# Performance work log

Hardware: AMD Instinct MI355X
Metric: run time of the kernel (lower is better)

## Reference

```python
import jax, jax.numpy as jnp
import numpy as np

N = 10000        # nodes
E = 160000       # graph edges (avg degree 16)
EI = 100000      # interaction edges
EP = 50000       # positive interaction edges
EA = 50000       # a2b edges
H, D = 4, 128    # GAT heads, per-head (and per-layer) dim
F_IN, F_EDGE = 39, 27   # 17+19+3 node feats, 27 edge feats
EMB = 256
FCN_IN = F_IN + 3 * D + D  # 551: x stacked with 3 GAT outputs + GCN output

PARAM_SHAPES = []
for l, fin in enumerate([F_IN, D, D]):
    PARAM_SHAPES += [(f"gat{l}_W", (fin, H * D)), (f"gat{l}_We", (F_EDGE, H * D)),
                     (f"gat{l}_asrc", (H, D)), (f"gat{l}_adst", (H, D)),
                     (f"gat{l}_aedge", (H, D)), (f"gat{l}_b", (D,))]
PARAM_SHAPES += [("gcn_W", (D, D)), ("gcn_b", (D,))]
for nm, fi, hh, fo in [("fcn", FCN_IN, 1024, EMB), ("link", 2 * EMB + 2, 1024, 1),
                       ("a2b", 2 * EMB, 1024, 6), ("node", EMB, 1024, 16),
                       ("int", 2 * EMB + 2, 1024, 3)]:
    PARAM_SHAPES += [(f"{nm}_W1", (fi, hh)), (f"{nm}_b1", (hh,)),
                     (f"{nm}_g", (hh,)), (f"{nm}_be", (hh,)),
                     (f"{nm}_W2", (hh, fo)), (f"{nm}_b2", (fo,))]
PARAM_NAMES = [n for n, _ in PARAM_SHAPES]


def setup_inputs():
    ks = jax.random.split(jax.random.key(0), len(PARAM_SHAPES) + 10)
    inp = {
        "x": jax.random.normal(ks[0], (N, F_IN), jnp.float32),
        "edge_index": jax.random.randint(ks[1], (2, E), 0, N),
        "edge_attr": jax.random.normal(ks[2], (E, F_EDGE), jnp.float32),
        "interaction_edge_index_pos": jax.random.randint(ks[3], (2, EP), 0, N),
        "interaction_edge_index": jax.random.randint(ks[4], (2, EI), 0, N),
        "xyz_data": jax.random.normal(ks[5], (N, 3), jnp.float32),
        "vector_data": jax.random.normal(ks[6], (N, 3), jnp.float32),
        "a2b_index": jax.random.randint(ks[7], (2, EA), 0, N),
        "mask": jnp.zeros((1,), jnp.float32),  # only used by the (disabled) evolver path
    }
    for i, (name, shp) in enumerate(PARAM_SHAPES):
        if name.endswith("_g"):
            inp[name] = jnp.ones(shp, jnp.float32)        # BatchNorm gamma
        elif name.endswith(("_be", "_b", "_b1", "_b2")):
            inp[name] = jnp.zeros(shp, jnp.float32)       # biases / BN beta
        else:
            inp[name] = jax.random.normal(ks[10 + i], shp, jnp.float32) * 0.05
    return inp


def _bn(h, g, b, eps=1e-5):
    # BatchNorm1d in training mode: biased batch statistics over axis 0
    m = h.mean(0)
    v = ((h - m) ** 2).mean(0)
    return (h - m) * jax.lax.rsqrt(v + eps) * g + b


def _seg_softmax(logits, seg, n):
    m = jax.ops.segment_max(logits, seg, num_segments=n)
    e = jnp.exp(logits - m[seg])
    s = jax.ops.segment_sum(e, seg, num_segments=n)
    return e / (s[seg] + 1e-16)


def _cos(a, b, eps=1e-8):
    na = jnp.maximum(jnp.sqrt((a * a).sum(1)), eps)
    nb = jnp.maximum(jnp.sqrt((b * b).sum(1)), eps)
    return (a * b).sum(1) / (na * nb)


def _forward(x, edge_attr, xyz_data, vector_data, edge_index, iep, iei, a2b_index, params):
    p = dict(zip(PARAM_NAMES, params))
    n = x.shape[0]
    src, dst = edge_index[0], edge_index[1]
    loops = jnp.arange(n)
    # GATConv add_self_loops with fill_value='mean': per-node mean of incoming edge_attr
    cnt = jax.ops.segment_sum(jnp.ones(src.shape[0], x.dtype), dst, num_segments=n)
    loop_attr = jax.ops.segment_sum(edge_attr, dst, num_segments=n) / jnp.maximum(cnt, 1.0)[:, None]
    src_a = jnp.concatenate([src, loops])
    dst_a = jnp.concatenate([dst, loops])
    ea_a = jnp.concatenate([edge_attr, loop_attr], 0)

    def gat(xx, W, We, asrc, adst, aedge, b):
        h = (xx @ W).reshape(n, H, D)
        a_s = (h * asrc).sum(-1)                               # [n,H]
        a_d = (h * adst).sum(-1)                               # [n,H]
        a_e = ((ea_a @ We).reshape(-1, H, D) * aedge).sum(-1)  # [E',H]
        alpha = jax.nn.leaky_relu(a_s[src_a] + a_d[dst_a] + a_e, 0.2)
        alpha = _seg_softmax(alpha, dst_a, n)                  # softmax over incoming edges
        out = jax.ops.segment_sum(h[src_a] * alpha[:, :, None], dst_a, num_segments=n)
        return out.mean(1) + b                                 # concat=False -> mean over heads

    out = x
    steps = [x]
    for l in range(3):
        out = jax.nn.relu(gat(out, p[f"gat{l}_W"], p[f"gat{l}_We"], p[f"gat{l}_asrc"],
                              p[f"gat{l}_adst"], p[f"gat{l}_aedge"], p[f"gat{l}_b"]))
        steps.append(out)
    # GCNConv: self loops (weight 1) + symmetric normalization
    deg = jax.ops.segment_sum(jnp.ones(dst_a.shape[0], x.dtype), dst_a, num_segments=n)
    dinv = jnp.where(deg > 0, deg ** -0.5, 0.0)
    norm = dinv[src_a] * dinv[dst_a]
    hg = out @ p["gcn_W"]
    out = jax.ops.segment_sum(hg[src_a] * norm[:, None], dst_a, num_segments=n) + p["gcn_b"]
    steps.append(out)

    feat = jnp.concatenate(steps, 1)                           # [n, 551]
    h = jax.nn.relu(feat @ p["fcn_W1"] + p["fcn_b1"])
    h = _bn(h, p["fcn_g"], p["fcn_be"])
    emb = jax.nn.relu(h @ p["fcn_W2"] + p["fcn_b2"])           # [n, 256]

    def head(z, nm):
        hh = jax.nn.relu(z @ p[f"{nm}_W1"] + p[f"{nm}_b1"])
        hh = _bn(hh, p[f"{nm}_g"], p[f"{nm}_be"])
        return hh @ p[f"{nm}_W2"] + p[f"{nm}_b2"]

    def pair_feat(idx):
        z = jnp.concatenate([emb[idx[0]], emb[idx[1]]], 1)
        d = ((xyz_data[idx[0]] - xyz_data[idx[1]]) ** 2).sum(1)  # squared distance (no sqrt)
        a = _cos(vector_data[idx[0]], vector_data[idx[1]])
        return jnp.concatenate([z, d[:, None], a[:, None]], 1)

    link_preds = head(pair_feat(iei), "link")
    a2b_preds = head(jnp.concatenate([emb[a2b_index[0]], emb[a2b_index[1]]], 1), "a2b")
    node_preds = head(emb, "node")
    int_preds = head(pair_feat(iep), "int")
    return (link_preds, a2b_preds, node_preds, int_preds)


def reference(x, edge_index, edge_attr, interaction_edge_index_pos, interaction_edge_index,
              xyz_data, vector_data, a2b_index, mask,
              gat0_W, gat0_We, gat0_asrc, gat0_adst, gat0_aedge, gat0_b,
              gat1_W, gat1_We, gat1_asrc, gat1_adst, gat1_aedge, gat1_b,
              gat2_W, gat2_We, gat2_asrc, gat2_adst, gat2_aedge, gat2_b,
              gcn_W, gcn_b,
              fcn_W1, fcn_b1, fcn_g, fcn_be, fcn_W2, fcn_b2,
              link_W1, link_b1, link_g, link_be, link_W2, link_b2,
              a2b_W1, a2b_b1, a2b_g, a2b_be, a2b_W2, a2b_b2,
              node_W1, node_b1, node_g, node_be, node_W2, node_b2,
              int_W1, int_b1, int_g, int_be, int_W2, int_b2):
    loc = locals()
    params = tuple(loc[nm] for nm in PARAM_NAMES)
    return _forward(x, edge_attr, xyz_data, vector_data, edge_index,
                    interaction_edge_index_pos, interaction_edge_index, a2b_index, params)
```

## Files before the change

### kernel.cpp

```cpp
#include <hip/hip_runtime.h>
#include <hip/hip_bf16.h>
#include <cstdint>
#include <cstddef>

typedef __attribute__((ext_vector_type(8))) short bf16x8;
typedef __attribute__((ext_vector_type(4))) float f32x4;

__device__ inline float bf2f(unsigned short u) {
    union { float f; unsigned int i; } c; c.i = ((unsigned int)u) << 16; return c.f;
}
__device__ inline unsigned short f2b(float v) {
    __hip_bfloat16 h = __float2bfloat16(v);
    union { __hip_bfloat16 b; unsigned short u; } c; c.b = h; return c.u;
}

__device__ inline float wmax64(float v) {
    #pragma unroll
    for (int o = 32; o; o >>= 1) v = fmaxf(v, __shfl_xor(v, o));
    return v;
}
__device__ inline float wsum64(float v) {
    #pragma unroll
    for (int o = 32; o; o >>= 1) v += __shfl_xor(v, o);
    return v;
// ... 156 lines not shown
        float l0 = a_s[s * 4 + 0] + d0 + a_e[(size_t)eid * 4 + 0];
        float l1 = a_s[s * 4 + 1] + d1 + a_e[(size_t)eid * 4 + 1];
        float l2 = a_s[s * 4 + 2] + d2 + a_e[(size_t)eid * 4 + 2];
        float l3 = a_s[s * 4 + 3] + d3 + a_e[(size_t)eid * 4 + 3];
        l0 = l0 > 0.f ? l0 : 0.2f * l0;
        l1 = l1 > 0.f ? l1 : 0.2f * l1;
        l2 = l2 > 0.f ? l2 : 0.2f * l2;
        l3 = l3 > 0.f ? l3 : 0.2f * l3;
        m0 = fmaxf(m0, l0); m1 = fmaxf(m1, l1); m2 = fmaxf(m2, l2); m3 = fmaxf(m3, l3);
    }
    m0 = wmax64(m0); m1 = wmax64(m1); m2 = wmax64(m2); m3 = wmax64(m3);
    float s0 = 0, s1 = 0, s2 = 0, s3 = 0;
    for (int e = lane; e < total; e += 64) {
        int eid, s;
        if (e < cnt) { eid = ceid[beg + e]; s = esrc[eid]; } else { eid = E_ + i; s = i; }
        float l0 = a_s[s * 4 + 0] + d0 + a_e[(size_t)eid * 4 + 0];
        float l1 = a_s[s * 4 + 1] + d1 + a_e[(size_t)eid * 4 + 1];
        float l2 = a_s[s * 4 + 2] + d2 + a_e[(size_t)eid * 4 + 2];
        float l3 = a_s[s * 4 + 3] + d3 + a_e[(size_t)eid * 4 + 3];
        l0 = l0 > 0.f ? l0 : 0.2f * l0;
        l1 = l1 > 0.f ? l1 : 0.2f * l1;
        l2 = l2 > 0.f ? l2 : 0.2f * l2;
        l3 = l3 > 0.f ? l3 : 0.2f * l3;
        s0 += __expf(l0 - m0); s1 += __expf(l1 - m1);
        s2 += __expf(l2 - m2); s3 += __expf(l3 - m3);
    }
    s0 = wsum64(s0); s1 = wsum64(s1); s2 = wsum64(s2); s3 = wsum64(s3);
    const int myh = lane >> 4;
    const float mm = myh == 0 ? m0 : myh == 1 ? m1 : myh == 2 ? m2 : m3;
    const float sv = myh == 0 ? s0 : myh == 1 ? s1 : myh == 2 ? s2 : s3;
    const float dd = myh == 0 ? d0 : myh == 1 ? d1 : myh == 2 ? d2 : d3;
    const float iv = 1.f / (sv + 1e-16f);
    float acc[8] = {0, 0, 0, 0, 0, 0, 0, 0};
    for (int e = 0; e < total; ++e) {
        int eid, s;
        if (e < cnt) { eid = ceid[beg + e]; s = esrc[eid]; } else { eid = E_ + i; s = i; }
        float l = a_s[s * 4 + myh] + dd + a_e[(size_t)eid * 4 + myh];
        l = l > 0.f ? l : 0.2f * l;
        const float wgt = __expf(l - mm) * iv;
        union { uint4 u; unsigned short us[8]; } c;
        c.u = *(const uint4*)(hb + (size_t)s * 512 + lane * 8);
        #pragma unroll
        for (int j = 0; j < 8; ++j) acc[j] += wgt * bf2f(c.us[j]);
    }
    __shared__ float sh[512];
    #pragma unroll
    for (int j = 0; j < 8; ++j) sh[lane * 8 + j] = acc[j];
    __syncthreads();
    #pragma unroll
    for (int r = 0; r < 2; ++r) {
        int d = lane * 2 + r;
        float v = 0.25f * (sh[d] + sh[128 + d] + sh[256 + d] + sh[384 + d]) + bvec[d];
        feat[(size_t)i * 551 + colofs + d] = fmaxf(v, 0.f);
    }
}

__global__ __launch_bounds__(64) void k_gcn(const unsigned short* __restrict__ hg, const int* __restrict__ esrc,
    const int* __restrict__ coff, const int* __restrict__ ceid, const int* __restrict__ indeg,
    const float* __restrict__ bvec, float* __restrict__ feat) {
    const int i = blockIdx.x;
    const int lane = threadIdx.x;
    const int beg = coff[i];
    const int cnt = coff[i + 1] - beg;
    const float di = rsqrtf((float)(indeg[i] + 1));
    const int d = lane * 2;
    unsigned int u0 = *(const unsigned int*)(hg + (size_t)i * 128 + d);
    float acc0 = bf2f((unsigned short)(u0 & 0xffff)) * di;
    float acc1 = bf2f((unsigned short)(u0 >> 16)) * di;
    for (int e = 0; e < cnt; ++e) {
        int eid = ceid[beg + e];
        int s = esrc[eid];
        float ds = rsqrtf((float)(indeg[s] + 1));
        unsigned int u = *(const unsigned int*)(hg + (size_t)s * 128 + d);
        acc0 += bf2f((unsigned short)(u & 0xffff)) * ds;
// ... 119 lines not shown
    for (int ch = 0; ch < nch; ++ch) {
        s += tmp[(size_t)ch * 2048 + c];
        ss += tmp[(size_t)ch * 2048 + 1024 + c];
    }
    float m = s / (float)M;
    float v = ss / (float)M - m * m;
    mv[c] = m;
    mv[1024 + c] = fmaxf(v, 0.f);
}

__global__ __launch_bounds__(256) void k_fold(const float* __restrict__ W2, const float* __restrict__ g,
    const float* __restrict__ be, const float* __restrict__ b2, const float* __restrict__ mv,
    float* __restrict__ W2f, float* __restrict__ b2f, int NO) {
    const int c = blockIdx.x;
    const int t = threadIdx.x;
    __shared__ float red[256];
    float accb = 0.f;
    for (int k = t; k < 1024; k += 256) {
        float s = (1.f / sqrtf(mv[1024 + k] + 1e-5f)) * g[k];
        float wv = W2[(size_t)k * NO + c];
        W2f[(size_t)k * NO + c] = wv * s;
        accb += (be[k] - mv[k] * s) * wv;
    }
    red[t] = accb;
    __syncthreads();
    for (int o = 128; o; o >>= 1) {
        if (t < o) red[t] += red[t + o];
        __syncthreads();
    }
    if (t == 0) b2f[c] = b2[c] + red[0];
}

template<bool HASEX>
__global__ __launch_bounds__(256) void k_pairA(
    const unsigned short* __restrict__ u0, const unsigned short* __restrict__ u1, int ldu,
    const float* __restrict__ b1, const float* __restrict__ W1ex,
    const int4* __restrict__ spp,
    int P, float* __restrict__ part) {
    const int b = blockIdx.x, t = threadIdx.x;
    const int chunk = (P + 1023) / 1024;
    const int r0 = b * chunk;
    const int r1 = min(P, r0 + chunk);
    const float4 bb = *(const float4*)(b1 + t * 4);
    float4 wd = make_float4(0, 0, 0, 0), wa = make_float4(0, 0, 0, 0);
    if constexpr (HASEX) {
        wd = *(const float4*)(W1ex + t * 4);
        wa = *(const float4*)(W1ex + 1024 + t * 4);
    }
    float s[4] = {0, 0, 0, 0}, ss[4] = {0, 0, 0, 0};
    int r = r0;
    for (; r + 1 < r1; r += 2) {
        const int4 rA = spp[r], rB = spp[r + 1];
        const int i0A = rA.x, i1A = rA.y, i0B = rB.x, i1B = rB.y;
        float dA = 0, aA = 0, dB = 0, aB = 0;
        if constexpr (HASEX) {
            dA = __int_as_float(rA.z); aA = __int_as_float(rA.w);
            dB = __int_as_float(rB.z); aB = __int_as_float(rB.w);
        }
        const ushort4 q0A = *(const ushort4*)(u0 + (size_t)i0A * ldu + t * 4);
        const ushort4 q1A = *(const ushort4*)(u1 + (size_t)i1A * ldu + t * 4);
        const ushort4 q0B = *(const ushort4*)(u0 + (size_t)i0B * ldu + t * 4);
        const ushort4 q1B = *(const ushort4*)(u1 + (size_t)i1B * ldu + t * 4);
        float hA[4], hB[4];
        hA[0] = bf2f(q0A.x) + bf2f(q1A.x) + bb.x;
        hA[1] = bf2f(q0A.y) + bf2f(q1A.y) + bb.y;
        hA[2] = bf2f(q0A.z) + bf2f(q1A.z) + bb.z;
        hA[3] = bf2f(q0A.w) + bf2f(q1A.w) + bb.w;
        hB[0] = bf2f(q0B.x) + bf2f(q1B.x) + bb.x;
        hB[1] = bf2f(q0B.y) + bf2f(q1B.y) + bb.y;
        hB[2] = bf2f(q0B.z) + bf2f(q1B.z) + bb.z;
        hB[3] = bf2f(q0B.w) + bf2f(q1B.w) + bb.w;
        if constexpr (HASEX) {
            hA[0] += dA * wd.x + aA * wa.x; hA[1] += dA * wd.y + aA * wa.y;
            hA[2] += dA * wd.z + aA * wa.z; hA[3] += dA * wd.w + aA * wa.w;
            hB[0] += dB * wd.x + aB * wa.x; hB[1] += dB * wd.y + aB * wa.y;
            hB[2] += dB * wd.z + aB * wa.z; hB[3] += dB * wd.w + aB * wa.w;
        }
        #pragma unroll
        for (int j = 0; j < 4; ++j) {
            float hvA = fmaxf(hA[j], 0.f);
            float hvB = fmaxf(hB[j], 0.f);
            s[j] += hvA + hvB; ss[j] += hvA * hvA + hvB * hvB;
        }
    }
    if (r < r1) {
        const int4 rA = spp[r];
        const int i0 = rA.x, i1 = rA.y;
        float d = 0, a = 0;
        if constexpr (HASEX) { d = __int_as_float(rA.z); a = __int_as_float(rA.w); }
        const ushort4 q0 = *(const ushort4*)(u0 + (size_t)i0 * ldu + t * 4);
        const ushort4 q1 = *(const ushort4*)(u1 + (size_t)i1 * ldu + t * 4);
        float h[4];
        h[0] = bf2f(q0.x) + bf2f(q1.x) + bb.x;
        h[1] = bf2f(q0.y) + bf2f(q1.y) + bb.y;
        h[2] = bf2f(q0.z) + bf2f(q1.z) + bb.z;
        h[3] = bf2f(q0.w) + bf2f(q1.w) + bb.w;
        if constexpr (HASEX) {
            h[0] += d * wd.x + a * wa.x; h[1] += d * wd.y + a * wa.y;
            h[2] += d * wd.z + a * wa.z; h[3] += d * wd.w + a * wa.w;
        }
        #pragma unroll
        for (int j = 0; j < 4; ++j) {
            float hv = fmaxf(h[j], 0.f);
            s[j] += hv; ss[j] += hv * hv;
        }
    }
    #pragma unroll
    for (int j = 0; j < 4; ++j) {
        part[(size_t)b * 2048 + t * 4 + j] = s[j];
        part[(size_t)b * 2048 + 1024 + t * 4 + j] = ss[j];
    }
}

template<int NO, bool HASEX>
__global__ __launch_bounds__(256) void k_pairB(
    const unsigned short* __restrict__ u0, const unsigned short* __restrict__ u1, int ldu,
    const float* __restrict__ b1, const float* __restrict__ W1ex,
    const float* __restrict__ W2f, const float* __restrict__ b2f,
    const int4* __restrict__ spp, const int* __restrict__ sord,
    float* __restrict__ out, int P) {
    const int t = threadIdx.x;
    const int wid = t >> 6, lane = t & 63;
    const int p0 = (blockIdx.x * 4 + wid) * 2;
    if (p0 >= P) return;
    const int p1 = p0 + 1;
    const bool has1 = p1 < P;
    const int4 rA = spp[p0];
    const int4 rB = spp[has1 ? p1 : p0];
    const int i0A = rA.x, i1A = rA.y, i0B = rB.x, i1B = rB.y;
    float dA = 0, aA = 0, dB = 0, aB = 0;
    if constexpr (HASEX) {
        dA = __int_as_float(rA.z); aA = __int_as_float(rA.w);
        dB = __int_as_float(rB.z); aB = __int_as_float(rB.w);
    }
    const int k0 = lane * 16;
    union U { uint4 u; unsigned short us[8]; };
    U a0A, a1A, b0A, b1A_, a0B, a1B, b0B, b1B_;
    const unsigned short* pa = u0 + (size_t)i0A * ldu + k0;
    const unsigned short* pb = u1 + (size_t)i1A * ldu + k0;
    const unsigned short* pc = u0 + (size_t)i0B * ldu + k0;
    const unsigned short* pd = u1 + (size_t)i1B * ldu + k0;
    a0A.u = *(const uint4*)(pa);     a1A.u = *(const uint4*)(pa + 8);
    b0A.u = *(const uint4*)(pb);     b1A_.u = *(const uint4*)(pb + 8);
    a0B.u = *(const uint4*)(pc);     a1B.u = *(const uint4*)(pc + 8);
    b0B.u = *(const uint4*)(pd);     b1B_.u = *(const uint4*)(pd + 8);
    float4 bbv[4];
    #pragma unroll
    for (int q = 0; q < 4; ++q) bbv[q] = *(const float4*)(b1 + k0 + q * 4);
    float4 wdv[4], wav[4];
    if constexpr (HASEX) {
        #pragma unroll
        for (int q = 0; q < 4; ++q) {
            wdv[q] = *(const float4*)(W1ex + k0 + q * 4);
            wav[q] = *(const float4*)(W1ex + 1024 + k0 + q * 4);
        }
    }
    float accA[NO], accB[NO];
    #pragma unroll
    for (int no = 0; no < NO; ++no) { accA[no] = 0.f; accB[no] = 0.f; }
    #pragma unroll
    for (int j = 0; j < 16; ++j) {
        const int q = j >> 2, c = j & 3;
        const float bbj = (&bbv[q].x)[c];
        float exA = 0.f, exB = 0.f;
        if constexpr (HASEX) {
            const float wdj = (&wdv[q].x)[c], waj = (&wav[q].x)[c];
            exA = dA * wdj + aA * waj;
            exB = dB * wdj + aB * waj;
        }
        const float hAv = (j < 8 ? bf2f(a0A.us[j]) : bf2f(a1A.us[j - 8]))
                        + (j < 8 ? bf2f(b0A.us[j]) : bf2f(b1A_.us[j - 8])) + bbj + exA;
        const float hBv = (j < 8 ? bf2f(a0B.us[j]) : bf2f(a1B.us[j - 8]))
                        + (j < 8 ? bf2f(b0B.us[j]) : bf2f(b1B_.us[j - 8])) + bbj + exB;
        const float rAv = fmaxf(hAv, 0.f);
        const float rBv = fmaxf(hBv, 0.f);
        const int kk = k0 + j;
        #pragma unroll
        for (int no = 0; no < NO; ++no) {
            const float wv = W2f[(size_t)kk * NO + no];
            accA[no] += rAv * wv;
            accB[no] += rBv * wv;
        }
    }
    const int oA = sord[p0];
    const int oB = has1 ? sord[p1] : 0;
    #pragma unroll
    for (int no = 0; no < NO; ++no) {
        float vA = accA[no], vB = accB[no];
        #pragma unroll
        for (int o = 32; o; o >>= 1) { vA += __shfl_down(vA, o); vB += __shfl_down(vB, o); }
        if (lane == 0) {
            out[(size_t)oA * NO + no] = vA + b2f[no];
            if (has1) out[(size_t)oB * NO + no] = vB + b2f[no];
        }
    }
}

extern "C" void kernel_launch(void* const* d_in, const int* in_sizes, int n_in,
                              void* d_out, int out_size, void* d_ws, size_t ws_size,
                              hipStream_t stream) {
    (void)n_in; (void)out_size; (void)ws_size;
    const float* x     = (const float*)d_in[0];
    const int*   eidx  = (const int*)d_in[1];
    const float* eattr = (const float*)d_in[2];
    const int*   iep   = (const int*)d_in[3];
    const int*   iei   = (const int*)d_in[4];
    const float* xyz   = (const float*)d_in[5];
    const float* vecd  = (const float*)d_in[6];
    const int*   a2bi  = (const int*)d_in[7];

    const int n   = in_sizes[0] / 39;
    const int E_  = in_sizes[1] / 2;
    const int EPn = in_sizes[3] / 2;
    const int EIn = in_sizes[4] / 2;
    const int EAn = in_sizes[7] / 2;
    const int Mp  = (n + 127) & ~127;
    const int MB  = (n + 127) / 128;

    const float* gatW[3]  = {(const float*)d_in[9],  (const float*)d_in[15], (const float*)d_in[21]};
    const float* gatWe[3] = {(const float*)d_in[10], (const float*)d_in[16], (const float*)d_in[22]};
    const float* gatAs[3] = {(const float*)d_in[11], (const float*)d_in[17], (const float*)d_in[23]};
    const float* gatAd[3] = {(const float*)d_in[12], (const float*)d_in[18], (const float*)d_in[24]};
    const float* gatAe[3] = {(const float*)d_in[13], (const float*)d_in[19], (const float*)d_in[25]};
    const float* gatB[3]  = {(const float*)d_in[14], (const float*)d_in[20], (const float*)d_in[26]};
    const float* gcnW = (const float*)d_in[27];
    const float* gcnB = (const float*)d_in[28];
    const float* fcnW1 = (const float*)d_in[29];
    const float* fcnB1 = (const float*)d_in[30];
    const float* fcnG  = (const float*)d_in[31];
    const float* fcnBe = (const float*)d_in[32];
    const float* fcnW2 = (const float*)d_in[33];
    const float* fcnB2 = (const float*)d_in[34];

    struct HeadP { const float *W1, *b1, *g, *be, *W2, *b2; };
    HeadP hp[4];
    for (int hh = 0; hh < 4; ++hh) {
        int base = 35 + hh * 6;
        hp[hh] = {(const float*)d_in[base], (const float*)d_in[base + 1], (const float*)d_in[base + 2],
                  (const float*)d_in[base + 3], (const float*)d_in[base + 4], (const float*)d_in[base + 5]};
    }

    char* w = (char*)d_ws;
    size_t off = 0;
    auto alloc = [&](size_t bytes) -> void* {
        void* p = w + off;
        off = (off + bytes + 255) & ~(size_t)255;
        return p;
    };
    int* indeg   = (int*)alloc((size_t)n * 4);
    int* fill    = (int*)alloc((size_t)n * 4);
    int* coff    = (int*)alloc((size_t)(n + 1) * 4);
    int* ceid    = (int*)alloc((size_t)E_ * 4);
    int* pcnt    = (int*)alloc((size_t)n * 4);
    int* pfill   = (int*)alloc((size_t)n * 4);
    int* poff    = (int*)alloc((size_t)(n + 1) * 4);
    int4* spp    = (int4*)alloc((size_t)EIn * 16);
    int* sord    = (int*)alloc((size_t)EIn * 4);
    float* lattr = (float*)alloc((size_t)n * 27 * 4);
    float* Wea   = (float*)alloc(27 * 4 * 4);
    float* a_e   = (float*)alloc((size_t)(E_ + n) * 4 * 4);
    float* a_s   = (float*)alloc((size_t)n * 4 * 4);
    float* a_d   = (float*)alloc((size_t)n * 4 * 4);
    float* part  = (float*)alloc((size_t)1024 * 2048 * 4);
    float* tmp   = (float*)alloc((size_t)32 * 2048 * 4);
    float* mv    = (float*)alloc(2048 * 4);
    float* W2f   = (float*)alloc((size_t)1024 * 256 * 4);
    float* b2f   = (float*)alloc(256 * 4);
    float* feat  = (float*)alloc((size_t)n * 551 * 4);
    unsigned short* hb   = (unsigned short*)alloc((size_t)n * 512 * 2);
    unsigned short* Ab   = (unsigned short*)alloc((size_t)Mp * 576 * 2);
    unsigned short* hidb = (unsigned short*)alloc((size_t)Mp * 1024 * 2);
    unsigned short* embb = (unsigned short*)alloc((size_t)Mp * 256 * 2);
    unsigned short* u01b = (unsigned short*)alloc((size_t)n * 2048 * 2);
    unsigned short* btB  = (unsigned short*)alloc((size_t)2048 * 256 * 2 > (size_t)1024 * 1024 * 2 ? (size_t)2048 * 1024 * 2 : (size_t)2048 * 1024 * 2);

    hipMemsetAsync(indeg, 0, (size_t)n * 4, stream);
    hipMemsetAsync(fill, 0, (size_t)n * 4, stream);
    hipMemsetAsync(hidb + (size_t)n * 1024, 0, (size_t)(Mp - n) * 1024 * 2, stream);
    hipMemsetAsync(embb + (size_t)n * 256, 0, (size_t)(Mp - n) * 256 * 2, stream);

    const int NCH = 32;
    auto stats_finish = [&](int M, int NB) {
        dim3 g1(8, NCH);
        k_red1<<<g1, 256, 0, stream>>>(part, tmp, NB, NCH);
        k_red2<<<4, 256, 0, stream>>>(tmp, mv, M, NCH);
    };
    auto stageA = [&](const float* src, int lds, int colofs, int K, int Kp) {
        int tot = Mp * Kp;
        k_stage_a<<<(tot + 255) / 256, 256, 0, stream>>>(src, lds, colofs, Ab, Kp, n, K, Mp);
    };
    auto convBt = [&](const float* src, int ldn, int K, int Kp, int N, int Np) {
        int tot = Np * Kp;
        k_conv_bt<<<(tot + 255) / 256, 256, 0, stream>>>(src, ldn, btB, Kp, K, N, Np);
    };
    auto bucket_pairs = [&](const int* pidx, int P, bool hasex) {
        hipMemsetAsync(pcnt, 0, (size_t)n * 4, stream);
        hipMemsetAsync(pfill, 0, (size_t)n * 4, stream);
        k_count<<<(P + 255) / 256, 256, 0, stream>>>(pidx, pcnt, P);
        k_scan<<<1, 1024, 0, stream>>>(pcnt, poff, n);
        if (hasex)
            k_pack_sorted<true><<<(P + 255) / 256, 256, 0, stream>>>(pidx, xyz, vecd, poff, pfill, spp, sord, P);
        else
            k_pack_sorted<false><<<(P + 255) / 256, 256, 0, stream>>>(pidx, xyz, vecd, poff, pfill, spp, sord, P);
    };

    const int* dsta = eidx + E_;
    k_count<<<(E_ + 255) / 256, 256, 0, stream>>>(dsta, indeg, E_);
// ... 18 lines not shown
    {
        stageA(feat, 551, 295, 128, 128);
        convBt(gcnW, 128, 128, 128, 128, 128);
        dim3 g(1, MB);
        gemm_mfma<1, false, false><<<g, 256, 0, stream>>>(Ab, 128, btB, 128, nullptr, hb, 128, n, 128, 128);
        k_gcn<<<n, 64, 0, stream>>>(hb, eidx, coff, ceid, indeg, gcnB, feat);
    }
    {
        stageA(feat, 551, 0, 551, 576);
        convBt(fcnW1, 1024, 551, 576, 1024, 1024);
        dim3 g(8, MB);
        gemm_mfma<1, true, true><<<g, 256, 0, stream>>>(Ab, 576, btB, 576, fcnB1, hidb, 1024, n, 1024, 576);
        k_stats1b<<<256, 256, 0, stream>>>(hidb, n, part);
        stats_finish(n, 256);
        k_fold<<<256, 256, 0, stream>>>(fcnW2, fcnG, fcnBe, fcnB2, mv, W2f, b2f, 256);
        convBt(W2f, 256, 1024, 1024, 256, 256);
        dim3 g2(2, MB);
        gemm_mfma<1, true, true><<<g2, 256, 0, stream>>>(hidb, 1024, btB, 1024, b2f, embb, 256, n, 256, 1024);
    }

    float* out = (float*)d_out;
    float* out_link = out;
    float* out_a2b  = out + (size_t)EIn;
    float* out_node = out_a2b + (size_t)EAn * 6;
    float* out_int  = out_node + (size_t)n * 16;

    const dim3 gu2(16, MB);

    {
        k_conv_bt2<<<(2048 * 256 + 255) / 256, 256, 0, stream>>>(hp[0].W1, btB);
        gemm_mfma<1, false, false><<<gu2, 256, 0, stream>>>(embb, 256, btB, 256, nullptr, u01b, 2048, n, 2048, 256);
        const float* W1ex = hp[0].W1 + (size_t)512 * 1024;
        bucket_pairs(iei, EIn, true);
        k_pairA<true><<<1024, 256, 0, stream>>>(u01b, u01b + 1024, 2048, hp[0].b1, W1ex, spp, EIn, part);
        stats_finish(EIn, 1024);
        k_fold<<<1, 256, 0, stream>>>(hp[0].W2, hp[0].g, hp[0].be, hp[0].b2, mv, W2f, b2f, 1);
        k_pairB<1, true><<<(EIn + 7) / 8, 256, 0, stream>>>(u01b, u01b + 1024, 2048, hp[0].b1, W1ex, W2f, b2f, spp, sord, out_link, EIn);
    }
    {
        k_conv_bt2<<<(2048 * 256 + 255) / 256, 256, 0, stream>>>(hp[1].W1, btB);
        gemm_mfma<1, false, false><<<gu2, 256, 0, stream>>>(embb, 256, btB, 256, nullptr, u01b, 2048, n, 2048, 256);
        bucket_pairs(a2bi, EAn, false);
        k_pairA<false><<<1024, 256, 0, stream>>>(u01b, u01b + 1024, 2048, hp[1].b1, nullptr, spp, EAn, part);
        stats_finish(EAn, 1024);
        k_fold<<<6, 256, 0, stream>>>(hp[1].W2, hp[1].g, hp[1].be, hp[1].b2, mv, W2f, b2f, 6);
        k_pairB<6, false><<<(EAn + 7) / 8, 256, 0, stream>>>(u01b, u01b + 1024, 2048, hp[1].b1, nullptr, W2f, b2f, spp, sord, out_a2b, EAn);
    }
    {
        convBt(hp[2].W1, 1024, 256, 256, 1024, 1024);
        dim3 gu(8, MB);
        gemm_mfma<1, true, true><<<gu, 256, 0, stream>>>(embb, 256, btB, 256, hp[2].b1, hidb, 1024, n, 1024, 256);
        k_stats1b<<<256, 256, 0, stream>>>(hidb, n, part);
        stats_finish(n, 256);
        k_fold<<<16, 256, 0, stream>>>(hp[2].W2, hp[2].g, hp[2].be, hp[2].b2, mv, W2f, b2f, 16);
        convBt(W2f, 16, 1024, 1024, 16, 128);
        dim3 g2(1, MB);
        gemm_mfma<0, false, true><<<g2, 256, 0, stream>>>(hidb, 1024, btB, 1024, b2f, out_node, 16, n, 16, 1024);
    }
    {
        k_conv_bt2<<<(2048 * 256 + 255) / 256, 256, 0, stream>>>(hp[3].W1, btB);
        gemm_mfma<1, false, false><<<gu2, 256, 0, stream>>>(embb, 256, btB, 256, nullptr, u01b, 2048, n, 2048, 256);
        const float* W1ex = hp[3].W1 + (size_t)512 * 1024;
        bucket_pairs(iep, EPn, true);
        k_pairA<true><<<1024, 256, 0, stream>>>(u01b, u01b + 1024, 2048, hp[3].b1, W1ex, spp, EPn, part);
        stats_finish(EPn, 1024);
        k_fold<<<3, 256, 0, stream>>>(hp[3].W2, hp[3].g, hp[3].be, hp[3].b2, mv, W2f, b2f, 3);
        k_pairB<3, true><<<(EPn + 7) / 8, 256, 0, stream>>>(u01b, u01b + 1024, 2048, hp[3].b1, W1ex, W2f, b2f, spp, sord, out_int, EPn);
    }
}
```

Measured before the change: 1.180 ms.

## Process pair heads per source-node bucket to reuse source row and weights

The pair-head stats and output kernels now assign one wavefront per source-node bucket, given by poff offsets from the existing bucketing. Each wavefront loads the source row of u0 once, adds the bias, and keeps W2 weights in registers. It then streams the destination rows for that bucket with a one-step software prefetch. This cuts redundant gathers of the source row and repeated W2 loads. The cost is load imbalance across buckets of different sizes and a larger partial-sum buffer, since NBK blocks now feed the reduction.

```diff
diff --git a/kernel.cpp b/kernel.cpp
--- a/kernel.cpp
+++ b/kernel.cpp
@@ -405,166 +405,142 @@
 }
 
 template<bool HASEX>
-__global__ __launch_bounds__(256) void k_pairA(
+__global__ __launch_bounds__(256) void k_pairA_bkt(
     const unsigned short* __restrict__ u0, const unsigned short* __restrict__ u1, int ldu,
     const float* __restrict__ b1, const float* __restrict__ W1ex,
-    const int4* __restrict__ spp,
-    int P, float* __restrict__ part) {
-    const int b = blockIdx.x, t = threadIdx.x;
-    const int chunk = (P + 1023) / 1024;
-    const int r0 = b * chunk;
-    const int r1 = min(P, r0 + chunk);
-    const float4 bb = *(const float4*)(b1 + t * 4);
-    float4 wd = make_float4(0, 0, 0, 0), wa = make_float4(0, 0, 0, 0);
-    if constexpr (HASEX) {
-        wd = *(const float4*)(W1ex + t * 4);
-        wa = *(const float4*)(W1ex + 1024 + t * 4);
-    }
-    float s[4] = {0, 0, 0, 0}, ss[4] = {0, 0, 0, 0};
-    int r = r0;
-    for (; r + 1 < r1; r += 2) {
-        const int4 rA = spp[r], rB = spp[r + 1];
-        const int i0A = rA.x, i1A = rA.y, i0B = rB.x, i1B = rB.y;
-        float dA = 0, aA = 0, dB = 0, aB = 0;
-        if constexpr (HASEX) {
-            dA = __int_as_float(rA.z); aA = __int_as_float(rA.w);
-            dB = __int_as_float(rB.z); aB = __int_as_float(rB.w);
-        }
-        const ushort4 q0A = *(const ushort4*)(u0 + (size_t)i0A * ldu + t * 4);
-        const ushort4 q1A = *(const ushort4*)(u1 + (size_t)i1A * ldu + t * 4);
-        const ushort4 q0B = *(const ushort4*)(u0 + (size_t)i0B * ldu + t * 4);
-        const ushort4 q1B = *(const ushort4*)(u1 + (size_t)i1B * ldu + t * 4);
-        float hA[4], hB[4];
-        hA[0] = bf2f(q0A.x) + bf2f(q1A.x) + bb.x;
-        hA[1] = bf2f(q0A.y) + bf2f(q1A.y) + bb.y;
-        hA[2] = bf2f(q0A.z) + bf2f(q1A.z) + bb.z;
-        hA[3] = bf2f(q0A.w) + bf2f(q1A.w) + bb.w;
-        hB[0] = bf2f(q0B.x) + bf2f(q1B.x) + bb.x;
-        hB[1] = bf2f(q0B.y) + bf2f(q1B.y) + bb.y;
-        hB[2] = bf2f(q0B.z) + bf2f(q1B.z) + bb.z;
-        hB[3] = bf2f(q0B.w) + bf2f(q1B.w) + bb.w;
-        if constexpr (HASEX) {
-            hA[0] += dA * wd.x + aA * wa.x; hA[1] += dA * wd.y + aA * wa.y;
-            hA[2] += dA * wd.z + aA * wa.z; hA[3] += dA * wd.w + aA * wa.w;
-            hB[0] += dB * wd.x + aB * wa.x; hB[1] += dB * wd.y + aB * wa.y;
-            hB[2] += dB * wd.z + aB * wa.z; hB[3] += dB * wd.w + aB * wa.w;
-        }
-        #pragma unroll
-        for (int j = 0; j < 4; ++j) {
-            float hvA = fmaxf(hA[j], 0.f);
-            float hvB = fmaxf(hB[j], 0.f);
-            s[j] += hvA + hvB; ss[j] += hvA * hvA + hvB * hvB;
-        }
-    }
-    if (r < r1) {
-        const int4 rA = spp[r];
-        const int i0 = rA.x, i1 = rA.y;
-        float d = 0, a = 0;
-        if constexpr (HASEX) { d = __int_as_float(rA.z); a = __int_as_float(rA.w); }
-        const ushort4 q0 = *(const ushort4*)(u0 + (size_t)i0 * ldu + t * 4);
-        const ushort4 q1 = *(const ushort4*)(u1 + (size_t)i1 * ldu + t * 4);
-        float h[4];
-        h[0] = bf2f(q0.x) + bf2f(q1.x) + bb.x;
-        h[1] = bf2f(q0.y) + bf2f(q1.y) + bb.y;
-        h[2] = bf2f(q0.z) + bf2f(q1.z) + bb.z;
-        h[3] = bf2f(q0.w) + bf2f(q1.w) + bb.w;
-        if constexpr (HASEX) {
-            h[0] += d * wd.x + a * wa.x; h[1] += d * wd.y + a * wa.y;
-            h[2] += d * wd.z + a * wa.z; h[3] += d * wd.w + a * wa.w;
-        }
-        #pragma unroll
-        for (int j = 0; j < 4; ++j) {
-            float hv = fmaxf(h[j], 0.f);
-            s[j] += hv; ss[j] += hv * hv;
-        }
-    }
-    #pragma unroll
-    for (int j = 0; j < 4; ++j) {
-        part[(size_t)b * 2048 + t * 4 + j] = s[j];
-        part[(size_t)b * 2048 + 1024 + t * 4 + j] = ss[j];
-    }
+    const int4* __restrict__ spp, const int* __restrict__ poff,
+    int nb, float* __restrict__ part) {
+    __shared__ float sacc[4][2048];
+    const int t = threadIdx.x;
+    const int wid = t >> 6, lane = t & 63;
+    const int k0 = lane * 16;
+    const int b = blockIdx.x * 4 + wid;
+    float s16[16], ss16[16];
+    #pragma unroll
+    for (int j = 0; j < 16; ++j) { s16[j] = 0.f; ss16[j] = 0.f; }
+    if (b < nb) {
+        const int beg = poff[b], end = poff[b + 1];
+        if (end > beg) {
+            union U { uint4 u; unsigned short us[8]; };
+            U c0, c1;
+            c0.u = *(const uint4*)(u0 + (size_t)b * ldu + k0);
+            c1.u = *(const uint4*)(u0 + (size_t)b * ldu + k0 + 8);
+            float base[16], wd[16], wa[16];
+            #pragma unroll
+            for (int j = 0; j < 16; ++j)
+                base[j] = bf2f(j < 8 ? c0.us[j] : c1.us[j - 8]) + b1[k0 + j];
+            if constexpr (HASEX) {
+                #pragma unroll
+                for (int j = 0; j < 16; ++j) {
+                    wd[j] = W1ex[k0 + j];
+                    wa[j] = W1ex[1024 + k0 + j];
+                }
+            }
+            int4 rec = spp[beg];
+            U n0, n1;
+            n0.u = *(const uint4*)(u1 + (size_t)rec.y * ldu + k0);
+            n1.u = *(const uint4*)(u1 + (size_t)rec.y * ldu + k0 + 8);
+            for (int p = beg; p < end; ++p) {
+                const int4 cur = rec;
+                const U m0 = n0, m1 = n1;
+                if (p + 1 < end) {
+                    rec = spp[p + 1];
+                    n0.u = *(const uint4*)(u1 + (size_t)rec.y * ldu + k0);
+                    n1.u = *(const uint4*)(u1 + (size_t)rec.y * ldu + k0 + 8);
+                }
+                float d = 0.f, a = 0.f;
+                if constexpr (HASEX) { d = __int_as_float(cur.z); a = __int_as_float(cur.w); }
+                #pragma unroll
+                for (int j = 0; j < 16; ++j) {
+                    float h = base[j] + bf2f(j < 8 ? m0.us[j] : m1.us[j - 8]);
+                    if constexpr (HASEX) h += d * wd[j] + a * wa[j];
+                    float r = fmaxf(h, 0.f);
+                    s16[j] += r; ss16[j] += r * r;
+                }
+            }
+        }
+    }
+    #pragma unroll
+    for (int j = 0; j < 16; ++j) {
+        sacc[wid][k0 + j] = s16[j];
+        sacc[wid][1024 + k0 + j] = ss16[j];
+    }
+    __syncthreads();
+    for (int c = t; c < 2048; c += 256)
+        part[(size_t)blockIdx.x * 2048 + c] = sacc[0][c] + sacc[1][c] + sacc[2][c] + sacc[3][c];
 }
 
 template<int NO, bool HASEX>
-__global__ __launch_bounds__(256) void k_pairB(
+__global__ __launch_bounds__(256) void k_pairB_bkt(
     const unsigned short* __restrict__ u0, const unsigned short* __restrict__ u1, int ldu,
     const float* __restrict__ b1, const float* __restrict__ W1ex,
     const float* __restrict__ W2f, const float* __restrict__ b2f,
-    const int4* __restrict__ spp, const int* __restrict__ sord,
-    float* __restrict__ out, int P) {
+    const int4* __restrict__ spp, const int* __restrict__ sord, const int* __restrict__ poff,
+    int nb, float* __restrict__ out) {
     const int t = threadIdx.x;
     const int wid = t >> 6, lane = t & 63;
-    const int p0 = (blockIdx.x * 4 + wid) * 2;
-    if (p0 >= P) return;
-    const int p1 = p0 + 1;
-    const bool has1 = p1 < P;
-    const int4 rA = spp[p0];
-    const int4 rB = spp[has1 ? p1 : p0];
-    const int i0A = rA.x, i1A = rA.y, i0B = rB.x, i1B = rB.y;
-    float dA = 0, aA = 0, dB = 0, aB = 0;
-    if constexpr (HASEX) {
-        dA = __int_as_float(rA.z); aA = __int_as_float(rA.w);
-        dB = __int_as_float(rB.z); aB = __int_as_float(rB.w);
-    }
+    const int b = blockIdx.x * 4 + wid;
+    if (b >= nb) return;
+    const int beg = poff[b], end = poff[b + 1];
+    if (end <= beg) return;
     const int k0 = lane * 16;
     union U { uint4 u; unsigned short us[8]; };
-    U a0A, a1A, b0A, b1A_, a0B, a1B, b0B, b1B_;
-    const unsigned short* pa = u0 + (size_t)i0A * ldu + k0;
-    const unsigned short* pb = u1 + (size_t)i1A * ldu + k0;
-    const unsigned short* pc = u0 + (size_t)i0B * ldu + k0;
-    const unsigned short* pd = u1 + (size_t)i1B * ldu + k0;
-    a0A.u = *(const uint4*)(pa);     a1A.u = *(const uint4*)(pa + 8);
-    b0A.u = *(const uint4*)(pb);     b1A_.u = *(const uint4*)(pb + 8);
-    a0B.u = *(const uint4*)(pc);     a1B.u = *(const uint4*)(pc + 8);
-    b0B.u = *(const uint4*)(pd);     b1B_.u = *(const uint4*)(pd + 8);
-    float4 bbv[4];
-    #pragma unroll
-    for (int q = 0; q < 4; ++q) bbv[q] = *(const float4*)(b1 + k0 + q * 4);
-    float4 wdv[4], wav[4];
+    U c0, c1;
+    c0.u = *(const uint4*)(u0 + (size_t)b * ldu + k0);
+    c1.u = *(const uint4*)(u0 + (size_t)b * ldu + k0 + 8);
+    float base[16], wd[16], wa[16];
+    #pragma unroll
+    for (int j = 0; j < 16; ++j)
+        base[j] = bf2f(j < 8 ? c0.us[j] : c1.us[j - 8]) + b1[k0 + j];
     if constexpr (HASEX) {
         #pragma unroll
-        for (int q = 0; q < 4; ++q) {
-            wdv[q] = *(const float4*)(W1ex + k0 + q * 4);
-            wav[q] = *(const float4*)(W1ex + 1024 + k0 + q * 4);
-        }
-    }
-    float accA[NO], accB[NO];
-    #pragma unroll
-    for (int no = 0; no < NO; ++no) { accA[no] = 0.f; accB[no] = 0.f; }
-    #pragma unroll
-    for (int j = 0; j < 16; ++j) {
-        const int q = j >> 2, c = j & 3;
-        const float bbj = (&bbv[q].x)[c];
-        float exA = 0.f, exB = 0.f;
-        if constexpr (HASEX) {
-            const float wdj = (&wdv[q].x)[c], waj = (&wav[q].x)[c];
-            exA = dA * wdj + aA * waj;
-            exB = dB * wdj + aB * waj;
-        }
-        const float hAv = (j < 8 ? bf2f(a0A.us[j]) : bf2f(a1A.us[j - 8]))
-                        + (j < 8 ? bf2f(b0A.us[j]) : bf2f(b1A_.us[j - 8])) + bbj + exA;
-        const float hBv = (j < 8 ? bf2f(a0B.us[j]) : bf2f(a1B.us[j - 8]))
-                        + (j < 8 ? bf2f(b0B.us[j]) : bf2f(b1B_.us[j - 8])) + bbj + exB;
-        const float rAv = fmaxf(hAv, 0.f);
-        const float rBv = fmaxf(hBv, 0.f);
-        const int kk = k0 + j;
+        for (int j = 0; j < 16; ++j) {
+            wd[j] = W1ex[k0 + j];
+            wa[j] = W1ex[1024 + k0 + j];
+        }
+    }
+    float w2l[16][NO];
+    #pragma unroll
+    for (int j = 0; j < 16; ++j)
+        #pragma unroll
+        for (int no = 0; no < NO; ++no)
+            w2l[j][no] = W2f[(size_t)(k0 + j) * NO + no];
+    float b2l[NO];
+    #pragma unroll
+    for (int no = 0; no < NO; ++no) b2l[no] = b2f[no];
+
+    int4 rec = spp[beg];
+    U n0, n1;
+    n0.u = *(const uint4*)(u1 + (size_t)rec.y * ldu + k0);
+    n1.u = *(const uint4*)(u1 + (size_t)rec.y * ldu + k0 + 8);
+    for (int p = beg; p < end; ++p) {
+        const int4 cur = rec;
+        const U m0 = n0, m1 = n1;
+        if (p + 1 < end) {
+            rec = spp[p + 1];
+            n0.u = *(const uint4*)(u1 + (size_t)rec.y * ldu + k0);
+            n1.u = *(const uint4*)(u1 + (size_t)rec.y * ldu + k0 + 8);
+        }
+        float d = 0.f, a = 0.f;
+        if constexpr (HASEX) { d = __int_as_float(cur.z); a = __int_as_float(cur.w); }
+        float acc[NO];
+        #pragma unroll
+        for (int no = 0; no < NO; ++no) acc[no] = 0.f;
+        #pragma unroll
+        for (int j = 0; j < 16; ++j) {
+            float h = base[j] + bf2f(j < 8 ? m0.us[j] : m1.us[j - 8]);
+            if constexpr (HASEX) h += d * wd[j] + a * wa[j];
+            const float r = fmaxf(h, 0.f);
+            #pragma unroll
+            for (int no = 0; no < NO; ++no) acc[no] += r * w2l[j][no];
+        }
+        const int orow = sord[p];
         #pragma unroll
         for (int no = 0; no < NO; ++no) {
-            const float wv = W2f[(size_t)kk * NO + no];
-            accA[no] += rAv * wv;
-            accB[no] += rBv * wv;
-        }
-    }
-    const int oA = sord[p0];
-    const int oB = has1 ? sord[p1] : 0;
-    #pragma unroll
-    for (int no = 0; no < NO; ++no) {
-        float vA = accA[no], vB = accB[no];
-        #pragma unroll
-        for (int o = 32; o; o >>= 1) { vA += __shfl_down(vA, o); vB += __shfl_down(vB, o); }
-        if (lane == 0) {
-            out[(size_t)oA * NO + no] = vA + b2f[no];
-            if (has1) out[(size_t)oB * NO + no] = vB + b2f[no];
+            float v = acc[no];
+            #pragma unroll
+            for (int o = 32; o; o >>= 1) v += __shfl_down(v, o);
+            if (lane == 0) out[(size_t)orow * NO + no] = v + b2l[no];
         }
     }
 }
@@ -589,6 +565,7 @@
     const int EAn = in_sizes[7] / 2;
     const int Mp  = (n + 127) & ~127;
     const int MB  = (n + 127) / 128;
+    const int NBK = (n + 3) / 4;
 
     const float* gatW[3]  = {(const float*)d_in[9],  (const float*)d_in[15], (const float*)d_in[21]};
     const float* gatWe[3] = {(const float*)d_in[10], (const float*)d_in[16], (const float*)d_in[22]};
@@ -634,7 +611,7 @@
     float* a_e   = (float*)alloc((size_t)(E_ + n) * 4 * 4);
     float* a_s   = (float*)alloc((size_t)n * 4 * 4);
     float* a_d   = (float*)alloc((size_t)n * 4 * 4);
-    float* part  = (float*)alloc((size_t)1024 * 2048 * 4);
+    float* part  = (float*)alloc((size_t)2560 * 2048 * 4);
     float* tmp   = (float*)alloc((size_t)32 * 2048 * 4);
     float* mv    = (float*)alloc(2048 * 4);
     float* W2f   = (float*)alloc((size_t)1024 * 256 * 4);
@@ -645,7 +622,7 @@
     unsigned short* hidb = (unsigned short*)alloc((size_t)Mp * 1024 * 2);
     unsigned short* embb = (unsigned short*)alloc((size_t)Mp * 256 * 2);
     unsigned short* u01b = (unsigned short*)alloc((size_t)n * 2048 * 2);
-    unsigned short* btB  = (unsigned short*)alloc((size_t)2048 * 256 * 2 > (size_t)1024 * 1024 * 2 ? (size_t)2048 * 1024 * 2 : (size_t)2048 * 1024 * 2);
+    unsigned short* btB  = (unsigned short*)alloc((size_t)2048 * 1024 * 2);
 
     hipMemsetAsync(indeg, 0, (size_t)n * 4, stream);
     hipMemsetAsync(fill, 0, (size_t)n * 4, stream);
@@ -730,19 +707,19 @@
         gemm_mfma<1, false, false><<<gu2, 256, 0, stream>>>(embb, 256, btB, 256, nullptr, u01b, 2048, n, 2048, 256);
         const float* W1ex = hp[0].W1 + (size_t)512 * 1024;
         bucket_pairs(iei, EIn, true);
-        k_pairA<true><<<1024, 256, 0, stream>>>(u01b, u01b + 1024, 2048, hp[0].b1, W1ex, spp, EIn, part);
-        stats_finish(EIn, 1024);
+        k_pairA_bkt<true><<<NBK, 256, 0, stream>>>(u01b, u01b + 1024, 2048, hp[0].b1, W1ex, spp, poff, n, part);
+        stats_finish(EIn, NBK);
         k_fold<<<1, 256, 0, stream>>>(hp[0].W2, hp[0].g, hp[0].be, hp[0].b2, mv, W2f, b2f, 1);
-        k_pairB<1, true><<<(EIn + 7) / 8, 256, 0, stream>>>(u01b, u01b + 1024, 2048, hp[0].b1, W1ex, W2f, b2f, spp, sord, out_link, EIn);
+        k_pairB_bkt<1, true><<<NBK, 256, 0, stream>>>(u01b, u01b + 1024, 2048, hp[0].b1, W1ex, W2f, b2f, spp, sord, poff, n, out_link);
     }
     {
         k_conv_bt2<<<(2048 * 256 + 255) / 256, 256, 0, stream>>>(hp[1].W1, btB);
         gemm_mfma<1, false, false><<<gu2, 256, 0, stream>>>(embb, 256, btB, 256, nullptr, u01b, 2048, n, 2048, 256);
         bucket_pairs(a2bi, EAn, false);
-        k_pairA<false><<<1024, 256, 0, stream>>>(u01b, u01b + 1024, 2048, hp[1].b1, nullptr, spp, EAn, part);
-        stats_finish(EAn, 1024);
+        k_pairA_bkt<false><<<NBK, 256, 0, stream>>>(u01b, u01b + 1024, 2048, hp[1].b1, nullptr, spp, poff, n, part);
+        stats_finish(EAn, NBK);
         k_fold<<<6, 256, 0, stream>>>(hp[1].W2, hp[1].g, hp[1].be, hp[1].b2, mv, W2f, b2f, 6);
-        k_pairB<6, false><<<(EAn + 7) / 8, 256, 0, stream>>>(u01b, u01b + 1024, 2048, hp[1].b1, nullptr, W2f, b2f, spp, sord, out_a2b, EAn);
+        k_pairB_bkt<6, false><<<NBK, 256, 0, stream>>>(u01b, u01b + 1024, 2048, hp[1].b1, nullptr, W2f, b2f, spp, sord, poff, n, out_a2b);
     }
     {
         convBt(hp[2].W1, 1024, 256, 256, 1024, 1024);
@@ -760,9 +737,9 @@
         gemm_mfma<1, false, false><<<gu2, 256, 0, stream>>>(embb, 256, btB, 256, nullptr, u01b, 2048, n, 2048, 256);
         const float* W1ex = hp[3].W1 + (size_t)512 * 1024;
         bucket_pairs(iep, EPn, true);
-        k_pairA<true><<<1024, 256, 0, stream>>>(u01b, u01b + 1024, 2048, hp[3].b1, W1ex, spp, EPn, part);
-        stats_finish(EPn, 1024);
+        k_pairA_bkt<true><<<NBK, 256, 0, stream>>>(u01b, u01b + 1024, 2048, hp[3].b1, W1ex, spp, poff, n, part);
+        stats_finish(EPn, NBK);
         k_fold<<<3, 256, 0, stream>>>(hp[3].W2, hp[3].g, hp[3].be, hp[3].b2, mv, W2f, b2f, 3);
-        k_pairB<3, true><<<(EPn + 7) / 8, 256, 0, stream>>>(u01b, u01b + 1024, 2048, hp[3].b1, W1ex, W2f, b2f, spp, sord, out_int, EPn);
-    }
-}
+        k_pairB_bkt<3, true><<<NBK, 256, 0, stream>>>(u01b, u01b + 1024, 2048, hp[3].b1, W1ex, W2f, b2f, spp, sord, poff, n, out_int);
+    }
+}
```

Result: slower. 1.248 ms (+5.8%).

## Process sorted pair chunks per wave and prefetch GAT aggregation rows

Applied to the files above, without the earlier changes.

The pair-head second stage now gives each wavefront a chunk of 16 sorted pairs instead of 2. Per-lane bias, extra weights and folded W2 are held in registers, and the source-node row plus bias is reused while consecutive pairs share the same first index. Loads of the four second-index rows are issued together. The GAT aggregation loop also software-prefetches the next edge's feature row. Together these cut redundant global loads and expose memory-level parallelism, at the cost of higher register pressure and fewer waves in flight.

```diff
diff --git a/kernel.cpp b/kernel.cpp
--- a/kernel.cpp
+++ b/kernel.cpp
@@ -212,14 +212,22 @@
     const float dd = myh == 0 ? d0 : myh == 1 ? d1 : myh == 2 ? d2 : d3;
     const float iv = 1.f / (sv + 1e-16f);
     float acc[8] = {0, 0, 0, 0, 0, 0, 0, 0};
+    int eidN, sN;
+    if (0 < cnt) { eidN = ceid[beg]; sN = esrc[eidN]; } else { eidN = E_ + i; sN = i; }
+    union HU { uint4 u; unsigned short us[8]; };
+    HU cN;
+    cN.u = *(const uint4*)(hb + (size_t)sN * 512 + lane * 8);
     for (int e = 0; e < total; ++e) {
-        int eid, s;
-        if (e < cnt) { eid = ceid[beg + e]; s = esrc[eid]; } else { eid = E_ + i; s = i; }
+        const int eid = eidN, s = sN;
+        const HU c = cN;
+        if (e + 1 < total) {
+            if (e + 1 < cnt) { eidN = ceid[beg + e + 1]; sN = esrc[eidN]; }
+            else { eidN = E_ + i; sN = i; }
+            cN.u = *(const uint4*)(hb + (size_t)sN * 512 + lane * 8);
+        }
         float l = a_s[s * 4 + myh] + dd + a_e[(size_t)eid * 4 + myh];
         l = l > 0.f ? l : 0.2f * l;
         const float wgt = __expf(l - mm) * iv;
-        union { uint4 u; unsigned short us[8]; } c;
-        c.u = *(const uint4*)(hb + (size_t)s * 512 + lane * 8);
         #pragma unroll
         for (int j = 0; j < 8; ++j) acc[j] += wgt * bf2f(c.us[j]);
     }
@@ -486,7 +494,7 @@
 }
 
 template<int NO, bool HASEX>
-__global__ __launch_bounds__(256) void k_pairB(
+__global__ __launch_bounds__(256) void k_pairB_chunk(
     const unsigned short* __restrict__ u0, const unsigned short* __restrict__ u1, int ldu,
     const float* __restrict__ b1, const float* __restrict__ W1ex,
     const float* __restrict__ W2f, const float* __restrict__ b2f,
@@ -494,77 +502,91 @@
     float* __restrict__ out, int P) {
     const int t = threadIdx.x;
     const int wid = t >> 6, lane = t & 63;
-    const int p0 = (blockIdx.x * 4 + wid) * 2;
-    if (p0 >= P) return;
-    const int p1 = p0 + 1;
-    const bool has1 = p1 < P;
-    const int4 rA = spp[p0];
-    const int4 rB = spp[has1 ? p1 : p0];
-    const int i0A = rA.x, i1A = rA.y, i0B = rB.x, i1B = rB.y;
-    float dA = 0, aA = 0, dB = 0, aB = 0;
+    const int c0 = (blockIdx.x * 4 + wid) * 16;
+    if (c0 >= P) return;
+    const int cend = min(P, c0 + 16);
+    const int k0 = lane * 16;
+    float bb[16], wd[16], wa[16];
+    #pragma unroll
+    for (int j = 0; j < 16; ++j) bb[j] = b1[k0 + j];
     if constexpr (HASEX) {
-        dA = __int_as_float(rA.z); aA = __int_as_float(rA.w);
-        dB = __int_as_float(rB.z); aB = __int_as_float(rB.w);
-    }
-    const int k0 = lane * 16;
+        #pragma unroll
+        for (int j = 0; j < 16; ++j) {
+            wd[j] = W1ex[k0 + j];
+            wa[j] = W1ex[1024 + k0 + j];
+        }
+    }
+    float w2l[16][NO];
+    #pragma unroll
+    for (int j = 0; j < 16; ++j)
+        #pragma unroll
+        for (int no = 0; no < NO; ++no)
+            w2l[j][no] = W2f[(size_t)(k0 + j) * NO + no];
+    float b2l[NO];
+    #pragma unroll
+    for (int no = 0; no < NO; ++no) b2l[no] = b2f[no];
+
     union U { uint4 u; unsigned short us[8]; };
-    U a0A, a1A, b0A, b1A_, a0B, a1B, b0B, b1B_;
-    const unsigned short* pa = u0 + (size_t)i0A * ldu + k0;
-    const unsigned short* pb = u1 + (size_t)i1A * ldu + k0;
-    const unsigned short* pc = u0 + (size_t)i0B * ldu + k0;
-    const unsigned short* pd = u1 + (size_t)i1B * ldu + k0;
-    a0A.u = *(const uint4*)(pa);     a1A.u = *(const uint4*)(pa + 8);
-    b0A.u = *(const uint4*)(pb);     b1A_.u = *(const uint4*)(pb + 8);
-    a0B.u = *(const uint4*)(pc);     a1B.u = *(const uint4*)(pc + 8);
-    b0B.u = *(const uint4*)(pd);     b1B_.u = *(const uint4*)(pd + 8);
-    float4 bbv[4];
-    #pragma unroll
-    for (int q = 0; q < 4; ++q) bbv[q] = *(const float4*)(b1 + k0 + q * 4);
-    float4 wdv[4], wav[4];
-    if constexpr (HASEX) {
+    int held = -1;
+    float base[16];
+    for (int g0 = c0; g0 < cend; g0 += 4) {
+        int4 rec0, rec1, rec2, rec3;
+        U m00, m01, m10, m11, m20, m21, m30, m31;
+        const int cnt = cend - g0;
+        rec0 = spp[g0];
+        m00.u = *(const uint4*)(u1 + (size_t)rec0.y * ldu + k0);
+        m01.u = *(const uint4*)(u1 + (size_t)rec0.y * ldu + k0 + 8);
+        if (cnt > 1) {
+            rec1 = spp[g0 + 1];
+            m10.u = *(const uint4*)(u1 + (size_t)rec1.y * ldu + k0);
+            m11.u = *(const uint4*)(u1 + (size_t)rec1.y * ldu + k0 + 8);
+        }
+        if (cnt > 2) {
+            rec2 = spp[g0 + 2];
+            m20.u = *(const uint4*)(u1 + (size_t)rec2.y * ldu + k0);
+            m21.u = *(const uint4*)(u1 + (size_t)rec2.y * ldu + k0 + 8);
+        }
+        if (cnt > 3) {
+            rec3 = spp[g0 + 3];
+            m30.u = *(const uint4*)(u1 + (size_t)rec3.y * ldu + k0);
+            m31.u = *(const uint4*)(u1 + (size_t)rec3.y * ldu + k0 + 8);
+        }
         #pragma unroll
         for (int q = 0; q < 4; ++q) {
-            wdv[q] = *(const float4*)(W1ex + k0 + q * 4);
-            wav[q] = *(const float4*)(W1ex + 1024 + k0 + q * 4);
-        }
-    }
-    float accA[NO], accB[NO];
-    #pragma unroll
-    for (int no = 0; no < NO; ++no) { accA[no] = 0.f; accB[no] = 0.f; }
-    #pragma unroll
-    for (int j = 0; j < 16; ++j) {
-        const int q = j >> 2, c = j & 3;
-        const float bbj = (&bbv[q].x)[c];
-        float exA = 0.f, exB = 0.f;
-        if constexpr (HASEX) {
-            const float wdj = (&wdv[q].x)[c], waj = (&wav[q].x)[c];
-            exA = dA * wdj + aA * waj;
-            exB = dB * wdj + aB * waj;
-        }
-        const float hAv = (j < 8 ? bf2f(a0A.us[j]) : bf2f(a1A.us[j - 8]))
-                        + (j < 8 ? bf2f(b0A.us[j]) : bf2f(b1A_.us[j - 8])) + bbj + exA;
-        const float hBv = (j < 8 ? bf2f(a0B.us[j]) : bf2f(a1B.us[j - 8]))
-                        + (j < 8 ? bf2f(b0B.us[j]) : bf2f(b1B_.us[j - 8])) + bbj + exB;
-        const float rAv = fmaxf(hAv, 0.f);
-        const float rBv = fmaxf(hBv, 0.f);
-        const int kk = k0 + j;
-        #pragma unroll
-        for (int no = 0; no < NO; ++no) {
-            const float wv = W2f[(size_t)kk * NO + no];
-            accA[no] += rAv * wv;
-            accB[no] += rBv * wv;
-        }
-    }
-    const int oA = sord[p0];
-    const int oB = has1 ? sord[p1] : 0;
-    #pragma unroll
-    for (int no = 0; no < NO; ++no) {
-        float vA = accA[no], vB = accB[no];
-        #pragma unroll
-        for (int o = 32; o; o >>= 1) { vA += __shfl_down(vA, o); vB += __shfl_down(vB, o); }
-        if (lane == 0) {
-            out[(size_t)oA * NO + no] = vA + b2f[no];
-            if (has1) out[(size_t)oB * NO + no] = vB + b2f[no];
+            if (q >= cnt) break;
+            const int4 rec = (q == 0) ? rec0 : (q == 1) ? rec1 : (q == 2) ? rec2 : rec3;
+            const U mm0 = (q == 0) ? m00 : (q == 1) ? m10 : (q == 2) ? m20 : m30;
+            const U mm1 = (q == 0) ? m01 : (q == 1) ? m11 : (q == 2) ? m21 : m31;
+            if (rec.x != held) {
+                held = rec.x;
+                U c0u, c1u;
+                c0u.u = *(const uint4*)(u0 + (size_t)held * ldu + k0);
+                c1u.u = *(const uint4*)(u0 + (size_t)held * ldu + k0 + 8);
+                #pragma unroll
+                for (int j = 0; j < 16; ++j)
+                    base[j] = bf2f(j < 8 ? c0u.us[j] : c1u.us[j - 8]) + bb[j];
+            }
+            float d = 0.f, a = 0.f;
+            if constexpr (HASEX) { d = __int_as_float(rec.z); a = __int_as_float(rec.w); }
+            float acc[NO];
+            #pragma unroll
+            for (int no = 0; no < NO; ++no) acc[no] = 0.f;
+            #pragma unroll
+            for (int j = 0; j < 16; ++j) {
+                float h = base[j] + bf2f(j < 8 ? mm0.us[j] : mm1.us[j - 8]);
+                if constexpr (HASEX) h += d * wd[j] + a * wa[j];
+                const float r = fmaxf(h, 0.f);
+                #pragma unroll
+                for (int no = 0; no < NO; ++no) acc[no] += r * w2l[j][no];
+            }
+            const int orow = sord[g0 + q];
+            #pragma unroll
+            for (int no = 0; no < NO; ++no) {
+                float v = acc[no];
+                #pragma unroll
+                for (int o = 32; o; o >>= 1) v += __shfl_down(v, o);
+                if (lane == 0) out[(size_t)orow * NO + no] = v + b2l[no];
+            }
         }
     }
 }
@@ -645,7 +667,7 @@
     unsigned short* hidb = (unsigned short*)alloc((size_t)Mp * 1024 * 2);
     unsigned short* embb = (unsigned short*)alloc((size_t)Mp * 256 * 2);
     unsigned short* u01b = (unsigned short*)alloc((size_t)n * 2048 * 2);
-    unsigned short* btB  = (unsigned short*)alloc((size_t)2048 * 256 * 2 > (size_t)1024 * 1024 * 2 ? (size_t)2048 * 1024 * 2 : (size_t)2048 * 1024 * 2);
+    unsigned short* btB  = (unsigned short*)alloc((size_t)2048 * 1024 * 2);
 
     hipMemsetAsync(indeg, 0, (size_t)n * 4, stream);
     hipMemsetAsync(fill, 0, (size_t)n * 4, stream);
@@ -733,7 +755,7 @@
         k_pairA<true><<<1024, 256, 0, stream>>>(u01b, u01b + 1024, 2048, hp[0].b1, W1ex, spp, EIn, part);
         stats_finish(EIn, 1024);
         k_fold<<<1, 256, 0, stream>>>(hp[0].W2, hp[0].g, hp[0].be, hp[0].b2, mv, W2f, b2f, 1);
-        k_pairB<1, true><<<(EIn + 7) / 8, 256, 0, stream>>>(u01b, u01b + 1024, 2048, hp[0].b1, W1ex, W2f, b2f, spp, sord, out_link, EIn);
+        k_pairB_chunk<1, true><<<(EIn + 63) / 64, 256, 0, stream>>>(u01b, u01b + 1024, 2048, hp[0].b1, W1ex, W2f, b2f, spp, sord, out_link, EIn);
     }
     {
         k_conv_bt2<<<(2048 * 256 + 255) / 256, 256, 0, stream>>>(hp[1].W1, btB);
@@ -742,7 +764,7 @@
         k_pairA<false><<<1024, 256, 0, stream>>>(u01b, u01b + 1024, 2048, hp[1].b1, nullptr, spp, EAn, part);
         stats_finish(EAn, 1024);
         k_fold<<<6, 256, 0, stream>>>(hp[1].W2, hp[1].g, hp[1].be, hp[1].b2, mv, W2f, b2f, 6);
-        k_pairB<6, false><<<(EAn + 7) / 8, 256, 0, stream>>>(u01b, u01b + 1024, 2048, hp[1].b1, nullptr, W2f, b2f, spp, sord, out_a2b, EAn);
+        k_pairB_chunk<6, false><<<(EAn + 63) / 64, 256, 0, stream>>>(u01b, u01b + 1024, 2048, hp[1].b1, nullptr, W2f, b2f, spp, sord, out_a2b, EAn);
     }
     {
         convBt(hp[2].W1, 1024, 256, 256, 1024, 1024);
@@ -763,6 +785,6 @@
         k_pairA<true><<<1024, 256, 0, stream>>>(u01b, u01b + 1024, 2048, hp[3].b1, W1ex, spp, EPn, part);
         stats_finish(EPn, 1024);
         k_fold<<<3, 256, 0, stream>>>(hp[3].W2, hp[3].g, hp[3].be, hp[3].b2, mv, W2f, b2f, 3);
-        k_pairB<3, true><<<(EPn + 7) / 8, 256, 0, stream>>>(u01b, u01b + 1024, 2048, hp[3].b1, W1ex, W2f, b2f, spp, sord, out_int, EPn);
-    }
-}
+        k_pairB_chunk<3, true><<<(EPn + 63) / 64, 256, 0, stream>>>(u01b, u01b + 1024, 2048, hp[3].b1, W1ex, W2f, b2f, spp, sord, out_int, EPn);
+    }
+}
```

After: 1.199 ms. About the same (+1.6%).
